# Kernel optimization log

Hardware: AMD Instinct MI355X
Metric: run time of the kernel (lower is better)

The kernel has to match this reference:

```python
import jax, jax.numpy as jnp
import numpy as np

EPS = 1.1920929e-7  # torch.finfo(float32).eps, default for F.rms_norm
ATTN_SCALE = 0.1
ROPE_BASE = 10000.0


def _rms_norm(x):
    # F.rms_norm over last dim, no learned weight
    return x * jax.lax.rsqrt(jnp.mean(x * x, axis=-1, keepdims=True) + EPS)


def _rotary(x):
    # x: [B, T, H, D]; rotates halves as in the Rotary module
    T, D = x.shape[1], x.shape[3]
    half = D // 2
    inv_freq = 1.0 / (ROPE_BASE ** (jnp.arange(0, D, 2, dtype=jnp.float32) / D))  # [half]
    freqs = jnp.arange(T, dtype=jnp.float32)[:, None] * inv_freq[None, :]          # [T, half]
    cos = jnp.cos(freqs)[None, :, None, :]
    sin = jnp.sin(freqs)[None, :, None, :]
    x1, x2 = x[..., :half], x[..., half:]
    return jnp.concatenate([x1 * cos + x2 * sin, -x1 * sin + x2 * cos], axis=-1)


def setup_inputs() -> dict:
    key = jax.random.key(0)
    ks = jax.random.split(key, 8)
    B, T, dim, H, hd = 2, 2048, 1024, 16, 64
    gate_in = 12
    s = 1.0 / np.sqrt(dim)
    return {
        "x": jax.random.normal(ks[0], (B, T, dim), dtype=jnp.float32),
        "v1": jax.random.normal(ks[1], (B, T, H, hd), dtype=jnp.float32),
        "Wq": jax.random.uniform(ks[2], (dim, dim), jnp.float32, -s, s),
        "Wk": jax.random.uniform(ks[3], (dim, dim), jnp.float32, -s, s),
        "Wv": jax.random.uniform(ks[4], (dim, dim), jnp.float32, -s, s),
        "Wproj": jax.random.uniform(ks[5], (dim, dim), jnp.float32, -s, s),
        "Wg": jax.random.uniform(ks[6], (H, gate_in), jnp.float32,
                                  -1.0 / np.sqrt(gate_in), 1.0 / np.sqrt(gate_in)),
        "lamb": jnp.float32(0.5),
    }


def reference(x, v1, Wq, Wk, Wv, Wproj, Wg, lamb):
    B, T, dim = x.shape
    H, hd = v1.shape[2], v1.shape[3]
    q = (x @ Wq.T).reshape(B, T, H, hd)
    k = (x @ Wk.T).reshape(B, T, H, hd)
    v = (x @ Wv.T).reshape(B, T, H, hd)
    # value-residual mixing
    v = (1.0 - lamb) * v + lamb * v1
    # QK RMSNorm + RoPE
    q = _rotary(_rms_norm(q))
    k = _rotary(_rms_norm(k))
    # causal SDPA with fixed scale
    scores = jnp.einsum('bqhd,bkhd->bhqk', q, k) * ATTN_SCALE
    causal = jnp.tril(jnp.ones((T, T), dtype=bool))
    scores = jnp.where(causal[None, None], scores, jnp.float32(-jnp.inf))
    probs = jax.nn.softmax(scores, axis=-1)
    y = jnp.einsum('bhqk,bkhd->bqhd', probs, v)  # [B, T, H, hd]
    # sigmoid gate from first 12 channels of x
    gate = jax.nn.sigmoid(x[..., :Wg.shape[1]] @ Wg.T)  # [B, T, H]
    y = y * gate[..., None]
    y = y.reshape(B, T, H * hd) @ Wproj.T
    return y
```

## Files before the change

### kernel.cpp

```cpp
#include <hip/hip_runtime.h>
#include <math.h>


#define B_    2
#define T_    2048
#define DIM_  1024
#define H_    16
#define HD_   64
#define NROW  (B_ * T_)
#define EPS_  1.1920929e-07f
#define SCALE_ 0.1f
#define LOG2_10K 13.287712379549449f
#define INV2PI 0.15915494309189535f

typedef unsigned short u16;
typedef unsigned int   u32;
typedef __bf16 bf16x8 __attribute__((ext_vector_type(8)));
typedef __bf16 bf16x2 __attribute__((ext_vector_type(2)));
typedef float  f32x4  __attribute__((ext_vector_type(4)));

__device__ __forceinline__ u16 f2b(float f) {
  u32 u = __float_as_uint(f);
  u += 0x7fffu + ((u >> 16) & 1u);
  return (u16)(u >> 16);
}
__device__ __forceinline__ u32 pk2(float a, float b) {
#if __has_builtin(__builtin_amdgcn_cvt_pk_bf16_f32)
  bf16x2 r = __builtin_amdgcn_cvt_pk_bf16_f32(a, b);
  return __builtin_bit_cast(u32, r);
#else
  return (u32)f2b(a) | ((u32)f2b(b) << 16);
#endif
}
__device__ __forceinline__ void fast_sincos_rev(float rev, float* s, float* c) {
  const float r = rev - floorf(rev);
#if __has_builtin(__builtin_amdgcn_sinf) && __has_builtin(__builtin_amdgcn_cosf)
  *s = __builtin_amdgcn_sinf(r);
  *c = __builtin_amdgcn_cosf(r);
#else
  *s = __sinf(r * 6.283185307179586f);
  *c = __cosf(r * 6.283185307179586f);
#endif
}
#define MFMA16(a,b,c) __builtin_amdgcn_mfma_f32_16x16x32_bf16((a),(b),(c),0,0,0)

typedef const __attribute__((address_space(1))) unsigned char gbuf_t;
typedef __attribute__((address_space(3))) unsigned char lbuf_t;
__device__ __forceinline__ void gload_lds16(const u16* g, unsigned char* l) {
  __builtin_amdgcn_global_load_lds((gbuf_t*)g, (lbuf_t*)l, 16, 0, 0);
}

__global__ __launch_bounds__(256) void convert_all(
    const float* __restrict__ x, const float* __restrict__ Wq,
    const float* __restrict__ Wk, const float* __restrict__ Wv,
    const float* __restrict__ Wp,
    u16* __restrict__ xb, u16* __restrict__ wb ) {
  const int i = blockIdx.x * 256 + threadIdx.x;
  const float* src;
  u16* dst;
  int off;
  if (i < 1048576)       { src = x;  dst = xb;            off = i; }
  else if (i < 1310720)  { src = Wq; dst = wb;            off = i - 1048576; }
  else if (i < 1572864)  { src = Wk; dst = wb + 1048576;  off = i - 1310720; }
  else if (i < 1835008)  { src = Wv; dst = wb + 2097152;  off = i - 1572864; }
  else                   { src = Wp; dst = wb + 3145728;  off = i - 1835008; }
  const float4 f = ((const float4*)src)[off];
  uint2 o;
  o.x = pk2(f.x, f.y);
  o.y = pk2(f.z, f.w);
  ((uint2*)dst)[off] = o;
}

template <bool IS_PROJ>
__global__ __launch_bounds__(256) void gemm_rp(
    const u16* __restrict__ Ab, const u16* __restrict__ Wb,
    u16* __restrict__ qo, u16* __restrict__ ko, u16* __restrict__ vto,
    float* __restrict__ fo, const float* __restrict__ v1,
    const float* __restrict__ lambp) {
  __shared__ __attribute__((aligned(16))) unsigned char sm[32768];
  const int tid  = threadIdx.x;
  const int w    = tid >> 6;
  const int lane = tid & 63;
  const int lo = lane & 15, hi = lane >> 4;
  const int m0 = blockIdx.x << 7;
  const int by = blockIdx.y;
  const int mode = IS_PROJ ? 3 : (by >> 3);
  const int n0 = IS_PROJ ? (by << 7) : ((by & 7) << 7);
  const u16* W = IS_PROJ ? Wb : (Wb + (size_t)mode * (DIM_ * DIM_));

  const int wm = w & 1, wn = w >> 1;

  const u16* agA0 = Ab + (size_t)(m0 + (2 * w + 0) * 16 + lo) * DIM_ + (hi << 3);
  const u16* agA1 = Ab + (size_t)(m0 + (2 * w + 1) * 16 + lo) * DIM_ + (hi << 3);
  const u16* agB0 = W  + (size_t)(n0 + (2 * w + 0) * 16 + lo) * DIM_ + (hi << 3);
  const u16* agB1 = W  + (size_t)(n0 + (2 * w + 1) * 16 + lo) * DIM_ + (hi << 3);

  f32x4 acc[4][4];
#pragma unroll
  for (int i = 0; i < 4; ++i)
#pragma unroll
    for (int j = 0; j < 4; ++j) acc[i][j] = (f32x4){0.f, 0.f, 0.f, 0.f};

  {
    unsigned char* ad = sm + (2 * w) * 1024;
    unsigned char* bd = sm + 8192 + (2 * w) * 1024;
    gload_lds16(agA0, ad);
    gload_lds16(agA1, ad + 1024);
    gload_lds16(agB0, bd);
    gload_lds16(agB1, bd + 1024);
    agA0 += 32; agA1 += 32; agB0 += 32; agB1 += 32;
  }
  __syncthreads();

  int buf = 0;
  for (int kc = 0; kc < DIM_; kc += 32) {
    if (kc + 32 < DIM_) {
      unsigned char* ad = sm + ((buf ^ 1) << 14) + (2 * w) * 1024;
      unsigned char* bd = ad + 8192;
      gload_lds16(agA0, ad);
      gload_lds16(agA1, ad + 1024);
      gload_lds16(agB0, bd);
      gload_lds16(agB1, bd + 1024);
      agA0 += 32; agA1 += 32; agB0 += 32; agB1 += 32;
    }
    const unsigned char* Acur = sm + (buf << 14);
    const unsigned char* Bcur = Acur + 8192;
    bf16x8 bfr[4];
#pragma unroll
    for (int nt = 0; nt < 4; ++nt)
      bfr[nt] = *(const bf16x8*)(Bcur + (((wn * 4 + nt) * 64 + lane) << 4));
#pragma unroll
    for (int mt = 0; mt < 4; ++mt) {
      const bf16x8 af = *(const bf16x8*)(Acur + (((wm * 4 + mt) * 64 + lane) << 4));
#pragma unroll
      for (int nt = 0; nt < 4; ++nt)
        acc[mt][nt] = MFMA16(af, bfr[nt], acc[mt][nt]);
    }
    if (kc + 32 < DIM_) __syncthreads();
    buf ^= 1;
  }

  const int head = (n0 >> 6) + wn;
  if (mode <= 1) {
    u16* C = (mode == 0) ? qo : ko;
    const float if0 = exp2f(-(float)lo * (LOG2_10K / 32.f)) * INV2PI;
    const float if1 = exp2f(-(float)(lo + 16) * (LOG2_10K / 32.f)) * INV2PI;
#pragma unroll
    for (int mt = 0; mt < 4; ++mt)
#pragma unroll
      for (int r = 0; r < 4; ++r) {
        float ss = 0.f;
#pragma unroll
        for (int nt = 0; nt < 4; ++nt) { const float v = acc[mt][nt][r]; ss += v * v; }
        ss += __shfl_xor(ss, 1, 64); ss += __shfl_xor(ss, 2, 64);
        ss += __shfl_xor(ss, 4, 64); ss += __shfl_xor(ss, 8, 64);
        const float scl = rsqrtf(ss * (1.f / 64.f) + EPS_);
        const int row_g = m0 + wm * 64 + mt * 16 + hi * 4 + r;
        const float tpos = (float)(row_g & (T_ - 1));
        float sn0, cs0, sn1, cs1;
        fast_sincos_rev(tpos * if0, &sn0, &cs0);
        fast_sincos_rev(tpos * if1, &sn1, &cs1);
        u16* crow = C + (size_t)row_g * DIM_ + head * HD_;
        const float x10 = acc[mt][0][r] * scl, x11 = acc[mt][1][r] * scl;
        const float x20 = acc[mt][2][r] * scl, x21 = acc[mt][3][r] * scl;
        crow[lo]      = f2b(x10 * cs0 + x20 * sn0);
        crow[16 + lo] = f2b(x11 * cs1 + x21 * sn1);
        crow[32 + lo] = f2b(x20 * cs0 - x10 * sn0);
        crow[48 + lo] = f2b(x21 * cs1 - x11 * sn1);
      }
  } else if (mode == 2) {
    const float lam = lambp[0];
#pragma unroll
    for (int mt = 0; mt < 4; ++mt)
#pragma unroll
      for (int r = 0; r < 4; ++r) {
        const int row_g = m0 + wm * 64 + mt * 16 + hi * 4 + r;
        const int bb = row_g >> 11, tt = row_g & (T_ - 1);
        const int bh = bb * H_ + head;
        const float* v1r = v1 + (size_t)row_g * DIM_ + head * HD_;
#pragma unroll
        for (int nt = 0; nt < 4; ++nt) {
          const int d = nt * 16 + lo;
          const float ov = (1.f - lam) * acc[mt][nt][r] + lam * v1r[d];
          vto[((size_t)(bh * HD_ + d)) * T_ + tt] = f2b(ov);
        }
      }
  } else {
#pragma unroll
    for (int mt = 0; mt < 4; ++mt)
#pragma unroll
      for (int r = 0; r < 4; ++r) {
        const int row_g = m0 + wm * 64 + mt * 16 + hi * 4 + r;
        float* orow = fo + (size_t)row_g * DIM_ + n0 + wn * 64;
#pragma unroll
        for (int nt = 0; nt < 4; ++nt) orow[nt * 16 + lo] = acc[mt][nt][r];
      }
  }
}

__global__ __launch_bounds__(256) void gate_kernel(
    const float* __restrict__ x, const float* __restrict__ Wg,
    float* __restrict__ gate) {
  const int id = blockIdx.x * 256 + threadIdx.x;
  const int n = id >> 4, h = id & 15;
  const float* xr = x + (size_t)n * DIM_;
  const float* wr = Wg + h * 12;
  float s = 0.f;
#pragma unroll
  for (int j = 0; j < 12; ++j) s += xr[j] * wr[j];
  gate[id] = 1.f / (1.f + __expf(-s));
}

__global__ __launch_bounds__(256) void attn3(
    const u16* __restrict__ q, const u16* __restrict__ k, const u16* __restrict__ vt,
    const float* __restrict__ gate, u16* __restrict__ y) {
  __shared__ __attribute__((aligned(16))) unsigned char smem[16384];
  const int tid = threadIdx.x;
  const int wv = tid >> 6, lane = tid & 63, lo = lane & 15, hi = lane >> 4;
  const int idx = blockIdx.x;
  const int qt = 31 - (idx >> 5);
  const int bh = idx & 31;
  const int b = bh >> 4, h = bh & 15;
  const int qb = qt << 6;

  const int qrow = b * T_ + qb + wv * 16 + lo;
  const u16* qp = q + (size_t)qrow * DIM_ + h * HD_;
  const bf16x8 qf0 = *(const bf16x8*)(qp + hi * 8);
  const bf16x8 qf1 = *(const bf16x8*)(qp + 32 + hi * 8);

  f32x4 o[4];
#pragma unroll
  for (int i = 0; i < 4; ++i) o[i] = (f32x4){0.f, 0.f, 0.f, 0.f};
  float mrun = -1e30f, lrun = 0.f;

  const int sl = tid & 63, skh = (tid >> 6) & 1, st0 = tid >> 7;
  const int srow = sl & 15, skk = skh * 32 + ((sl >> 4) << 3);
  const u16* kg0 = k + ((size_t)(b * T_ + st0 * 16 + srow)) * DIM_ + h * HD_ + skk;
  const u16* kg1 = kg0 + (size_t)32 * DIM_;
  const u16* vg0 = vt + ((size_t)(bh * HD_ + st0 * 16 + srow)) * T_ + skk;
  const u16* vg1 = vg0 + (size_t)32 * T_;

  uint4 kr0 = *(const uint4*)kg0, kr1 = *(const uint4*)kg1;
  uint4 vr0 = *(const uint4*)vg0, vr1 = *(const uint4*)vg1;

  const int off0 = tid << 4, off1 = (tid + 256) << 4;

  for (int tix = 0; tix <= qt; ++tix) {
    __syncthreads();
    *(uint4*)(smem + off0) = kr0;
    *(uint4*)(smem + off1) = kr1;
    *(uint4*)(smem + 8192 + off0) = vr0;
    *(uint4*)(smem + 8192 + off1) = vr1;
    if (tix < qt) {
      const size_t ko = (size_t)(tix + 1) * 64 * DIM_;
      const size_t vo = (size_t)(tix + 1) * 64;
      kr0 = *(const uint4*)(kg0 + ko); kr1 = *(const uint4*)(kg1 + ko);
      vr0 = *(const uint4*)(vg0 + vo); vr1 = *(const uint4*)(vg1 + vo);
    }
    __syncthreads();

    f32x4 stl[4];
#pragma unroll
    for (int kt = 0; kt < 4; ++kt) stl[kt] = (f32x4){0.f, 0.f, 0.f, 0.f};
#pragma unroll
    for (int kh = 0; kh < 2; ++kh) {
      const bf16x8 qb_ = kh ? qf1 : qf0;
#pragma unroll
      for (int kt = 0; kt < 4; ++kt) {
        const bf16x8 af = *(const bf16x8*)(smem + (((kt * 2 + kh) * 64 + lane) << 4));
        stl[kt] = MFMA16(af, qb_, stl[kt]);
      }
    }
    const bool diag = (tix == qt);
#pragma unroll
    for (int kt = 0; kt < 4; ++kt)
#pragma unroll
      for (int r = 0; r < 4; ++r) {
        float s = stl[kt][r] * SCALE_;
        if (diag && (kt * 16 + hi * 4 + r > wv * 16 + lo)) s = -3e38f;
        stl[kt][r] = s;
      }
    float mx = stl[0][0];
#pragma unroll
    for (int kt = 0; kt < 4; ++kt)
#pragma unroll
      for (int r = 0; r < 4; ++r) mx = fmaxf(mx, stl[kt][r]);
    mx = fmaxf(mx, __shfl_xor(mx, 16, 64));
    mx = fmaxf(mx, __shfl_xor(mx, 32, 64));
    const float mn = fmaxf(mrun, mx);
    const float alpha = __expf(mrun - mn);
    mrun = mn;
    float ps = 0.f;
#pragma unroll
    for (int kt = 0; kt < 4; ++kt)
#pragma unroll
      for (int r = 0; r < 4; ++r) { stl[kt][r] = __expf(stl[kt][r] - mn); ps += stl[kt][r]; }
    ps += __shfl_xor(ps, 16, 64);
    ps += __shfl_xor(ps, 32, 64);
    lrun = lrun * alpha + ps;
#pragma unroll
    for (int dt = 0; dt < 4; ++dt) o[dt] *= alpha;

    u32 pkv[4][2];
#pragma unroll
    for (int kt = 0; kt < 4; ++kt) {
      pkv[kt][0] = pk2(stl[kt][0], stl[kt][1]);
      pkv[kt][1] = pk2(stl[kt][2], stl[kt][3]);
    }
#pragma unroll
    for (int kh = 0; kh < 2; ++kh) {
      uint4 w4;
      u32* w4p = (u32*)&w4;
#pragma unroll
      for (int wd = 0; wd < 4; ++wd) {
        const int src = (2 * (hi & 1) + (wd >> 1)) * 16 + lo;
        const u32 a  = (u32)__shfl((int)pkv[2 * kh][wd & 1], src, 64);
        const u32 bb = (u32)__shfl((int)pkv[2 * kh + 1][wd & 1], src, 64);
        w4p[wd] = (hi < 2) ? a : bb;
      }
      const bf16x8 pf = __builtin_bit_cast(bf16x8, w4);
#pragma unroll
      for (int dt = 0; dt < 4; ++dt) {
        const bf16x8 vf = *(const bf16x8*)(smem + 8192 + (((dt * 2 + kh) * 64 + lane) << 4));
        o[dt] = MFMA16(vf, pf, o[dt]);
      }
    }
  }

  const float inv = gate[(size_t)qrow * H_ + h] / lrun;
  u16* yrow = y + (size_t)qrow * DIM_ + h * HD_;
#pragma unroll
  for (int dt = 0; dt < 4; ++dt) {
    ushort4 pq;
    pq.x = f2b(o[dt][0] * inv); pq.y = f2b(o[dt][1] * inv);
    pq.z = f2b(o[dt][2] * inv); pq.w = f2b(o[dt][3] * inv);
    *(ushort4*)(yrow + dt * 16 + hi * 4) = pq;
  }
}

extern "C" void kernel_launch(void* const* d_in, const int* in_sizes, int n_in,
                              void* d_out, int out_size, void* d_ws, size_t ws_size,
                              hipStream_t stream) {
  const float* x    = (const float*)d_in[0];
  const float* v1   = (const float*)d_in[1];
  const float* Wq   = (const float*)d_in[2];
  const float* Wk   = (const float*)d_in[3];
  const float* Wv   = (const float*)d_in[4];
  const float* Wp   = (const float*)d_in[5];
  const float* Wg   = (const float*)d_in[6];
  const float* lamb = (const float*)d_in[7];

  const size_t NX = (size_t)NROW * DIM_;
  const size_t NW = (size_t)DIM_ * DIM_;

  u16* q  = (u16*)d_ws;
  u16* k  = q + NX;
  u16* vt = k + NX;
  u16* xb = vt + NX;
  u16* wb = xb + NX;
  float* gate = (float*)(wb + 4 * NW);

  const dim3 bb(256);

  convert_all<<<dim3(8192), bb, 0, stream>>>(x, Wq, Wk, Wv, Wp, xb, wb);
  gemm_rp<false><<<dim3(NROW / 128, 24), bb, 0, stream>>>(
      xb, wb, q, k, vt, nullptr, v1, lamb);
  gate_kernel<<<dim3(NROW * H_ / 256), bb, 0, stream>>>(x, Wg, gate);
  attn3<<<dim3(B_ * H_ * (T_ / 64)), bb, 0, stream>>>(q, k, vt, gate, q);
  gemm_rp<true><<<dim3(NROW / 128, 8), bb, 0, stream>>>(
      q, wb + 3 * NW, nullptr, nullptr, nullptr, (float*)d_out, nullptr, nullptr);
}
```

Before: 235.3 us.

## Triple-buffer GEMM LDS staging with vmcnt waits and single barrier per step

Changes the projection GEMM's shared-memory pipeline from double to triple buffering. Two k-chunks are prefetched up front, and each iteration waits with an explicit vmcnt count and one s_barrier instead of two __syncthreads. The goal is to keep more global-to-LDS loads in flight and hide their latency behind the MFMA work. LDS use per block grows from 32 KB to 48 KB, which may lower occupancy. Correctness now depends on the hand-written vmcnt accounting.

```diff
diff --git a/kernel.cpp b/kernel.cpp
--- a/kernel.cpp
+++ b/kernel.cpp
@@ -77,7 +77,7 @@
     u16* __restrict__ qo, u16* __restrict__ ko, u16* __restrict__ vto,
     float* __restrict__ fo, const float* __restrict__ v1,
     const float* __restrict__ lambp) {
-  __shared__ __attribute__((aligned(16))) unsigned char sm[32768];
+  __shared__ __attribute__((aligned(16))) unsigned char sm[49152];
   const int tid  = threadIdx.x;
   const int w    = tid >> 6;
   const int lane = tid & 63;
@@ -102,28 +102,40 @@
     for (int j = 0; j < 4; ++j) acc[i][j] = (f32x4){0.f, 0.f, 0.f, 0.f};
 
   {
-    unsigned char* ad = sm + (2 * w) * 1024;
-    unsigned char* bd = sm + 8192 + (2 * w) * 1024;
-    gload_lds16(agA0, ad);
-    gload_lds16(agA1, ad + 1024);
-    gload_lds16(agB0, bd);
-    gload_lds16(agB1, bd + 1024);
+    unsigned char* ad0 = sm + (2 * w) * 1024;
+    gload_lds16(agA0, ad0);
+    gload_lds16(agA1, ad0 + 1024);
+    gload_lds16(agB0, ad0 + 8192);
+    gload_lds16(agB1, ad0 + 9216);
     agA0 += 32; agA1 += 32; agB0 += 32; agB1 += 32;
-  }
-  __syncthreads();
-
-  int buf = 0;
+    unsigned char* ad1 = sm + 16384 + (2 * w) * 1024;
+    gload_lds16(agA0, ad1);
+    gload_lds16(agA1, ad1 + 1024);
+    gload_lds16(agB0, ad1 + 8192);
+    gload_lds16(agB1, ad1 + 9216);
+    agA0 += 32; agA1 += 32; agB0 += 32; agB1 += 32;
+  }
+
+  int cr = 0;
+  int cw = 2;
   for (int kc = 0; kc < DIM_; kc += 32) {
+    __builtin_amdgcn_sched_barrier(0);
     if (kc + 32 < DIM_) {
-      unsigned char* ad = sm + ((buf ^ 1) << 14) + (2 * w) * 1024;
-      unsigned char* bd = ad + 8192;
+      asm volatile("s_waitcnt vmcnt(4)" ::: "memory");
+    } else {
+      asm volatile("s_waitcnt vmcnt(0)" ::: "memory");
+    }
+    __builtin_amdgcn_s_barrier();
+    __builtin_amdgcn_sched_barrier(0);
+    if (kc + 64 < DIM_) {
+      unsigned char* ad = sm + cw * 16384 + (2 * w) * 1024;
       gload_lds16(agA0, ad);
       gload_lds16(agA1, ad + 1024);
-      gload_lds16(agB0, bd);
-      gload_lds16(agB1, bd + 1024);
+      gload_lds16(agB0, ad + 8192);
+      gload_lds16(agB1, ad + 9216);
       agA0 += 32; agA1 += 32; agB0 += 32; agB1 += 32;
     }
-    const unsigned char* Acur = sm + (buf << 14);
+    const unsigned char* Acur = sm + cr * 16384;
     const unsigned char* Bcur = Acur + 8192;
     bf16x8 bfr[4];
 #pragma unroll
@@ -136,8 +148,8 @@
       for (int nt = 0; nt < 4; ++nt)
         acc[mt][nt] = MFMA16(af, bfr[nt], acc[mt][nt]);
     }
-    if (kc + 32 < DIM_) __syncthreads();
-    buf ^= 1;
+    cr = (cr == 2) ? 0 : cr + 1;
+    cw = (cw == 2) ? 0 : cw + 1;
   }
 
   const int head = (n0 >> 6) + wn;
```

Result: faster. 226.3 us (-3.8%).
